# Kernel tuning notes

Measured on AMD Instinct MI355X. Metric: run time of the kernel, lower is better.

Reference implementation:

```python
import jax, jax.numpy as jnp
import numpy as np

L = 16
F = 2
N_MIN = 16.0
N_MAX = 524288.0
T = 524288  # 2**19
N_PTS = 2097152  # 2**21


def setup_inputs() -> dict:
    key = jax.random.key(0)
    k1, k2 = jax.random.split(key)
    x = jax.random.uniform(k1, (N_PTS,), dtype=jnp.float32, minval=-1.0, maxval=1.0)
    hash_table = jax.random.uniform(k2, (T, F), dtype=jnp.float32, minval=-0.001, maxval=0.001)
    return {"x": x, "hash_table": hash_table, "bound": 1}


def reference(x, hash_table, bound):
    # normalize coords to [0, 1]
    xn = (x + bound) / (2.0 * bound)
    # per-level geometric growth factor b
    b = jnp.exp((jnp.log(jnp.float32(N_MAX)) - jnp.log(jnp.float32(N_MIN))) / (L - 1))
    scales = N_MIN * b ** jnp.arange(L, dtype=jnp.float32) - 1.0  # [L]
    x_scaled = xn[:, None] * scales[None, :] + 0.5                # [N, L]
    indices = jnp.floor(x_scaled).astype(jnp.int32) % T           # [N, L]
    # gather per-level features and flatten: [N, L, F] -> [N, L*F]
    return hash_table[indices].reshape(x.shape[0], -1)
```

## Files before the change

kernel.cpp:

```cpp
#include <hip/hip_runtime.h>


constexpr int T_SIZE = 524288;
constexpr int N_PTS  = 2097152;
constexpr int SLOTS  = N_PTS * 8;
constexpr int KI     = 4;
constexpr int NTH    = SLOTS / KI;

typedef float vfloat4 __attribute__((ext_vector_type(4)));

__device__ __forceinline__ float scale_for_level(int l) {
    unsigned bits = ((130u + (unsigned)l) << 23)
                  | (0x800000u - (0x100000u >> l) - (unsigned)l);
    return __uint_as_float(bits);
}

__global__ __launch_bounds__(256) void hash_encode_kernel(
    const float* __restrict__ x,
    const float* __restrict__ table,
    const int* __restrict__ bound_p,
    float* __restrict__ out)
{
    int tid = blockIdx.x * 256 + threadIdx.x;

    int j  = tid & 7;
    int l0 = j << 1;
    float s0 = scale_for_level(l0);
    float s1 = scale_for_level(l0 + 1);

    float fb  = (float)bound_p[0];
    float fb2 = __fmul_rn(2.0f, fb);

    float xv[KI];
#pragma unroll
    for (int k = 0; k < KI; ++k) {
        int n = (tid + k * NTH) >> 3;
        xv[k] = __builtin_nontemporal_load(&x[n]);
    }

    int i0[KI], i1[KI];
#pragma unroll
    for (int k = 0; k < KI; ++k) {
        float xn  = __fdiv_rn(__fadd_rn(xv[k], fb), fb2);
        float xs0 = __fadd_rn(__fmul_rn(xn, s0), 0.5f);
        float xs1 = __fadd_rn(__fmul_rn(xn, s1), 0.5f);
        i0[k] = ((int)xs0) & (T_SIZE - 1);
        i1[k] = ((int)xs1) & (T_SIZE - 1);
    }

    const float2* t2 = (const float2*)table;
    float2 a[KI], b[KI];
#pragma unroll
    for (int k = 0; k < KI; ++k) {
        a[k] = t2[i0[k]];
        b[k] = t2[i1[k]];
    }

    vfloat4* o4 = (vfloat4*)out;
#pragma unroll
    for (int k = 0; k < KI; ++k) {
        vfloat4 o;
        o.x = a[k].x; o.y = a[k].y; o.z = b[k].x; o.w = b[k].y;
        o4[tid + k * NTH] = o;
    }
}

extern "C" void kernel_launch(void* const* d_in, const int* in_sizes, int n_in,
                              void* d_out, int out_size, void* d_ws, size_t ws_size,
                              hipStream_t stream) {
    const float* x     = (const float*)d_in[0];
    const float* table = (const float*)d_in[1];
    const int*   bound = (const int*)d_in[2];
    float* out = (float*)d_out;

    int blocks = NTH / 256;
    hash_encode_kernel<<<blocks, 256, 0, stream>>>(x, table, bound, out);
}
```

Measured before the change: 344.2 us.

## Stage low-level hash table entries in shared memory and use nontemporal stores

Each 1024-thread block copies the first 16384 table entries (128KB) into LDS. Lookups for the coarse levels, whose indices always fall inside that range, then read LDS instead of global memory. Work per thread doubles to eight slots, split into two groups of four, and output writes switch to nontemporal stores. The cost is a large per-block LDS copy, which is redundant across 2048 blocks and limits occupancy to one block per CU. There is also a divergent branch on level within each wavefront.

```diff
diff --git a/kernel.cpp b/kernel.cpp
--- a/kernel.cpp
+++ b/kernel.cpp
@@ -4,8 +4,10 @@
 constexpr int T_SIZE = 524288;
 constexpr int N_PTS  = 2097152;
 constexpr int SLOTS  = N_PTS * 8;
-constexpr int KI     = 4;
+constexpr int KI     = 8;
 constexpr int NTH    = SLOTS / KI;
+constexpr int BLK    = 1024;
+constexpr int LUT_N  = 16384;
 
 typedef float vfloat4 __attribute__((ext_vector_type(4)));
 
@@ -15,53 +17,73 @@
     return __uint_as_float(bits);
 }
 
-__global__ __launch_bounds__(256) void hash_encode_kernel(
+__global__ __launch_bounds__(BLK) void hash_encode_kernel(
     const float* __restrict__ x,
     const float* __restrict__ table,
     const int* __restrict__ bound_p,
     float* __restrict__ out)
 {
-    int tid = blockIdx.x * 256 + threadIdx.x;
+    __shared__ float2 lut[LUT_N];
 
+    {
+        const vfloat4* src = (const vfloat4*)table;
+        vfloat4*       dst = (vfloat4*)lut;
+#pragma unroll
+        for (int m = 0; m < LUT_N / 2 / BLK; ++m) {
+            int i4 = threadIdx.x + m * BLK;
+            dst[i4] = src[i4];
+        }
+    }
+
+    int tid = blockIdx.x * BLK + threadIdx.x;
     int j  = tid & 7;
-    int l0 = j << 1;
-    float s0 = scale_for_level(l0);
-    float s1 = scale_for_level(l0 + 1);
-
+    float s0 = scale_for_level(j << 1);
+    float s1 = scale_for_level((j << 1) + 1);
     float fb  = (float)bound_p[0];
     float fb2 = __fmul_rn(2.0f, fb);
 
-    float xv[KI];
-#pragma unroll
-    for (int k = 0; k < KI; ++k) {
-        int n = (tid + k * NTH) >> 3;
-        xv[k] = __builtin_nontemporal_load(&x[n]);
-    }
-
-    int i0[KI], i1[KI];
-#pragma unroll
-    for (int k = 0; k < KI; ++k) {
-        float xn  = __fdiv_rn(__fadd_rn(xv[k], fb), fb2);
-        float xs0 = __fadd_rn(__fmul_rn(xn, s0), 0.5f);
-        float xs1 = __fadd_rn(__fmul_rn(xn, s1), 0.5f);
-        i0[k] = ((int)xs0) & (T_SIZE - 1);
-        i1[k] = ((int)xs1) & (T_SIZE - 1);
-    }
+    __syncthreads();
 
     const float2* t2 = (const float2*)table;
-    float2 a[KI], b[KI];
+    vfloat4* o4 = (vfloat4*)out;
+
 #pragma unroll
-    for (int k = 0; k < KI; ++k) {
-        a[k] = t2[i0[k]];
-        b[k] = t2[i1[k]];
-    }
+    for (int g = 0; g < 2; ++g) {
+        float xv[4];
+#pragma unroll
+        for (int k = 0; k < 4; ++k) {
+            int slot = tid + (g * 4 + k) * NTH;
+            xv[k] = __builtin_nontemporal_load(&x[slot >> 3]);
+        }
 
-    vfloat4* o4 = (vfloat4*)out;
+        int i0[4], i1[4];
 #pragma unroll
-    for (int k = 0; k < KI; ++k) {
-        vfloat4 o;
-        o.x = a[k].x; o.y = a[k].y; o.z = b[k].x; o.w = b[k].y;
-        o4[tid + k * NTH] = o;
+        for (int k = 0; k < 4; ++k) {
+            float xn  = __fdiv_rn(__fadd_rn(xv[k], fb), fb2);
+            float xs0 = __fadd_rn(__fmul_rn(xn, s0), 0.5f);
+            float xs1 = __fadd_rn(__fmul_rn(xn, s1), 0.5f);
+            i0[k] = ((int)xs0) & (T_SIZE - 1);
+            i1[k] = ((int)xs1) & (T_SIZE - 1);
+        }
+
+        float2 a[4], b[4];
+        if (j <= 4) {
+#pragma unroll
+            for (int k = 0; k < 4; ++k) { a[k] = lut[i0[k]]; b[k] = lut[i1[k]]; }
+        } else if (j == 5) {
+#pragma unroll
+            for (int k = 0; k < 4; ++k) { a[k] = lut[i0[k]]; b[k] = t2[i1[k]]; }
+        } else {
+#pragma unroll
+            for (int k = 0; k < 4; ++k) { a[k] = t2[i0[k]]; b[k] = t2[i1[k]]; }
+        }
+
+#pragma unroll
+        for (int k = 0; k < 4; ++k) {
+            vfloat4 o;
+            o.x = a[k].x; o.y = a[k].y; o.z = b[k].x; o.w = b[k].y;
+            __builtin_nontemporal_store(o, o4 + (tid + (g * 4 + k) * NTH));
+        }
     }
 }
 
@@ -73,6 +95,6 @@
     const int*   bound = (const int*)d_in[2];
     float* out = (float*)d_out;
 
-    int blocks = NTH / 256;
-    hash_encode_kernel<<<blocks, 256, 0, stream>>>(x, table, bound, out);
+    int blocks = NTH / BLK;
+    hash_encode_kernel<<<blocks, BLK, 0, stream>>>(x, table, bound, out);
 }
```

Result: no change. 342.5 us (-0.5%).
